# Performance work log

Measured on AMD Instinct MI355X. Metric: run time of the kernel, lower is better.

The kernel has to match this reference:

```python
import jax, jax.numpy as jnp
import numpy as np

N_SPK, N_UTT, D_EMB = 1024, 20, 512
COS_EPS = 1e-8   # torch F.cosine_similarity default eps
SIM_EPS = 1e-6   # added to cosine and inside the log, per original code


def setup_inputs() -> dict:
    key = jax.random.key(0)
    embeddings = jax.random.normal(key, (N_SPK, N_UTT, D_EMB), dtype=jnp.float32)
    w = jnp.asarray(10.0, dtype=jnp.float32)
    b = jnp.asarray(-5.0, dtype=jnp.float32)
    return {"embeddings": embeddings, "w": w, "b": b}


def reference(embeddings, w, b):
    N, M, D = embeddings.shape
    sums = embeddings.sum(axis=1)                       # [N, D]
    centroids = sums / M                                # [N, D] full centroids
    cent_excl = (sums[:, None, :] - embeddings) / (M - 1)  # [N, M, D] leave-one-out

    def _norm(x):
        return x / jnp.maximum(jnp.linalg.norm(x, axis=-1, keepdims=True), COS_EPS)

    e_n = _norm(embeddings)          # [N, M, D]
    c_n = _norm(centroids)           # [N, D]
    ce_n = _norm(cent_excl)          # [N, M, D]

    # cosine vs every speaker centroid
    cs = jnp.einsum('nmd,kd->nmk', e_n, c_n)            # [N, M, N]
    # replace same-speaker column with leave-one-out cosine
    diag = jnp.sum(e_n * ce_n, axis=-1)                 # [N, M]
    same = jnp.eye(N, dtype=bool)[:, None, :]           # [N, 1, N]
    cossim = jnp.where(same, diag[:, :, None], cs) + SIM_EPS

    sim = w * cossim + b                                # [N, M, N]
    pos = w * (diag + SIM_EPS) + b                      # sim[j, i, j]
    lse = jnp.log(jnp.sum(jnp.exp(sim), axis=-1) + SIM_EPS)  # [N, M]
    loss = jnp.sum(lse - pos)
    return loss
```

## Files before the change

### kernel.cpp

```cpp
#include <hip/hip_runtime.h>
#include <hip/hip_bf16.h>

typedef unsigned short u16;
typedef unsigned int u32;
typedef unsigned char u8;
typedef int i32x8 __attribute__((ext_vector_type(8)));
typedef float f32x4 __attribute__((ext_vector_type(4)));

#define NSPK 1024
#define NUTT 20
#define DEMB 512
#define NROW (NSPK * NUTT)

__device__ __forceinline__ uint2 pk_fp8x8(float a, float b, float c, float d,
                                          float e, float f, float g, float h) {
    int lo = __builtin_amdgcn_cvt_pk_fp8_f32(a, b, 0, 0);
    lo = __builtin_amdgcn_cvt_pk_fp8_f32(c, d, lo, 1);
    int hi = __builtin_amdgcn_cvt_pk_fp8_f32(e, f, 0, 0);
    hi = __builtin_amdgcn_cvt_pk_fp8_f32(g, h, hi, 1);
    return make_uint2((u32)lo, (u32)hi);
}

__global__ __launch_bounds__(256) void prep_f(const float* __restrict__ E,
                                              u8* __restrict__ A,
                                              u8* __restrict__ Bc,
                                              float* __restrict__ diag,
                                              float* __restrict__ csd,
                                              float* __restrict__ out) {
    __shared__ float sbuf[4][DEMB];
    const int t = threadIdx.x, lane = t & 63, wv = t >> 6;
    const int n = blockIdx.x;
    const float* Eb = E + (size_t)n * (NUTT * DEMB) + (size_t)(wv * 5) * DEMB + lane * 8;

    float4 e0[5], e1[5];
    float4 p0 = {0, 0, 0, 0}, p1 = {0, 0, 0, 0};
#pragma unroll
    for (int i = 0; i < 5; ++i) {
        e0[i] = *(const float4*)(Eb + (size_t)i * DEMB);
        e1[i] = *(const float4*)(Eb + (size_t)i * DEMB + 4);
        p0.x += e0[i].x; p0.y += e0[i].y; p0.z += e0[i].z; p0.w += e0[i].w;
        p1.x += e1[i].x; p1.y += e1[i].y; p1.z += e1[i].z; p1.w += e1[i].w;
    }
    *(float4*)(&sbuf[wv][lane * 8])     = p0;
    *(float4*)(&sbuf[wv][lane * 8 + 4]) = p1;
    __syncthreads();

    float4 s0 = {0, 0, 0, 0}, s1 = {0, 0, 0, 0};
#pragma unroll
    for (int k = 0; k < 4; ++k) {
        float4 a = *(const float4*)(&sbuf[k][lane * 8]);
        float4 b = *(const float4*)(&sbuf[k][lane * 8 + 4]);
        s0.x += a.x; s0.y += a.y; s0.z += a.z; s0.w += a.w;
        s1.x += b.x; s1.y += b.y; s1.z += b.z; s1.w += b.w;
    }

    float ls = s0.x*s0.x + s0.y*s0.y + s0.z*s0.z + s0.w*s0.w
             + s1.x*s1.x + s1.y*s1.y + s1.z*s1.z + s1.w*s1.w;
#pragma unroll
    for (int o = 32; o; o >>= 1) ls += __shfl_xor(ls, o);
    const float ss = ls;
    const float rc = 1.0f / fmaxf(sqrtf(ss) * 0.05f, 1e-8f);
    const float g  = rc * 0.05f;

    ((uint2*)(Bc + (size_t)n * DEMB))[lane] =
        pk_fp8x8(s0.x * g, s0.y * g, s0.z * g, s0.w * g,
                 s1.x * g, s1.y * g, s1.z * g, s1.w * g);

#pragma unroll
    for (int i = 0; i < 5; ++i) {
        float ee = e0[i].x*e0[i].x + e0[i].y*e0[i].y + e0[i].z*e0[i].z + e0[i].w*e0[i].w
                 + e1[i].x*e1[i].x + e1[i].y*e1[i].y + e1[i].z*e1[i].z + e1[i].w*e1[i].w;
        float es = e0[i].x*s0.x + e0[i].y*s0.y + e0[i].z*s0.z + e0[i].w*s0.w
                 + e1[i].x*s1.x + e1[i].y*s1.y + e1[i].z*s1.z + e1[i].w*s1.w;
#pragma unroll
        for (int o = 32; o; o >>= 1) { ee += __shfl_xor(ee, o); es += __shfl_xor(es, o); }

        const float rne = 1.0f / fmaxf(sqrtf(ee), 1e-8f);
        const float pxx = ss - 2.f * es + ee;
        const float dg  = (es - ee) * rne / fmaxf(sqrtf(pxx), 1.9e-7f);

        const int r = n * NUTT + wv * 5 + i;
        ((uint2*)(A + (size_t)r * DEMB))[lane] =
            pk_fp8x8(e0[i].x * rne, e0[i].y * rne, e0[i].z * rne, e0[i].w * rne,
                     e1[i].x * rne, e1[i].y * rne, e1[i].z * rne, e1[i].w * rne);
        if (lane == 0) {
            diag[r] = dg;
            csd[r]  = es * g * rne;
        }
    }

    if (n == 0 && t == 0) out[0] = 0.f;
}

__device__ __forceinline__ void async_copy16(const void* g, void* l) {
    __builtin_amdgcn_global_load_lds(
        (const __attribute__((address_space(1))) void*)g,
        (__attribute__((address_space(3))) void*)l, 16, 0, 0);
}

__global__ __launch_bounds__(256, 1) void gemm_fin(const u8* __restrict__ A,
                                                   const u8* __restrict__ Bc,
                                                   const float* __restrict__ wp,
                                                   const float* __restrict__ bp,
                                                   const float* __restrict__ diag,
                                                   const float* __restrict__ csd,
                                                   float* __restrict__ out) {
    __shared__ u8 As[80 * DEMB];
    __shared__ u8 Bls[4][2][4096];
    __shared__ float red[4][80];
    __shared__ float s_red[4];
    const int t = threadIdx.x, lane = t & 63, wv = t >> 6;
    const int ml = lane & 15, q = lane >> 4;
    const int blk = blockIdx.x;
    const u8* Ag = A + (size_t)blk * 80 * DEMB;

    const float w = *wp, bb = *bp;

#pragma unroll
    for (int jj = 0; jj < 10; ++jj) {
        const int c = t + 256 * jj;
        const int r = c >> 5, sl = c & 31;
        async_copy16(Ag + (size_t)r * DEMB + ((sl ^ (r & 31)) << 4),
                     As + t * 16 + jj * 4096);
    }

    const int C0 = wv * 256;
    int rj[4], kg16[4];
#pragma unroll
    for (int j = 0; j < 4; ++j) {
        const int c = lane + 64 * j;
        rj[j] = c >> 3;
        kg16[j] = ((c & 7) ^ (rj[j] & 7)) << 4;
    }

#define STAGEB(U, KT, PAR)                                                    \
    {                                                                         \
        _Pragma("unroll")                                                     \
        for (int j = 0; j < 4; ++j)                                           \
            async_copy16(Bc + (size_t)(C0 + (U) * 32 + rj[j]) * DEMB +        \
                             (KT) * 128 + kg16[j],                            \
                         &Bls[wv][PAR][j * 1024 + lane * 16]);                \
    }

    STAGEB(0, 0, 0);
    STAGEB(0, 1, 1);
    asm volatile("s_waitcnt vmcnt(8)" ::: "memory");
    __builtin_amdgcn_sched_barrier(0);
    __builtin_amdgcn_s_barrier();
    __builtin_amdgcn_sched_barrier(0);

    i32x8 a[5][4];
#pragma unroll
    for (int m = 0; m < 5; ++m) {
        const int r = m * 16 + ml;
#pragma unroll
        for (int kt = 0; kt < 4; ++kt) {
            const int sl0 = (kt * 8 + 2 * q)     ^ (r & 31);
            const int sl1 = (kt * 8 + 2 * q + 1) ^ (r & 31);
            uint4 x = *(const uint4*)(As + r * DEMB + (sl0 << 4));
            uint4 y = *(const uint4*)(As + r * DEMB + (sl1 << 4));
            a[m][kt] = (i32x8){(int)x.x, (int)x.y, (int)x.z, (int)x.w,
                               (int)y.x, (int)y.y, (int)y.z, (int)y.w};
        }
    }

    f32x4 acc[5][2], rowpart[5];
#pragma unroll
    for (int m = 0; m < 5; ++m) {
        acc[m][0] = (f32x4){0.f, 0.f, 0.f, 0.f};
        acc[m][1] = (f32x4){0.f, 0.f, 0.f, 0.f};
        rowpart[m] = (f32x4){0.f, 0.f, 0.f, 0.f};
    }

    int bo0[2], bo1[2];
#pragma unroll
    for (int nf = 0; nf < 2; ++nf) {
        const int cc = nf * 16 + ml;
        bo0[nf] = cc * 128 + (((2 * q)     ^ (cc & 7)) << 4);
        bo1[nf] = cc * 128 + (((2 * q + 1) ^ (cc & 7)) << 4);
    }

    i32x8 bf[2][2];
#define LOADBF(PAR)                                                           \
    {                                                                         \
        _Pragma("unroll")                                                     \
        for (int nf = 0; nf < 2; ++nf) {                                      \
            uint4 x = *(const uint4*)(&Bls[wv][PAR][bo0[nf]]);                \
            uint4 y = *(const uint4*)(&Bls[wv][PAR][bo1[nf]]);                \
            bf[PAR][nf] = (i32x8){(int)x.x, (int)x.y, (int)x.z, (int)x.w,     \
                                  (int)y.x, (int)y.y, (int)y.z, (int)y.w};    \
        }                                                                     \
    }

    asm volatile("s_waitcnt vmcnt(4)" ::: "memory");
    __builtin_amdgcn_sched_barrier(0);
    LOADBF(0);

#pragma unroll
    for (int u = 0; u < 8; ++u) {
#pragma unroll
        for (int kt = 0; kt < 4; ++kt) {
            const int s = u * 4 + kt, par = s & 1;
            asm volatile("s_waitcnt lgkmcnt(0)" ::: "memory");
            __builtin_amdgcn_sched_barrier(0);
            if (s + 2 < 32) {
                const int s2 = s + 2;
                STAGEB(s2 >> 2, s2 & 3, par);
            }
            __builtin_amdgcn_sched_barrier(0);
            if (s == 30)      { asm volatile("s_waitcnt vmcnt(0)" ::: "memory"); }
            else if (s < 30)  { asm volatile("s_waitcnt vmcnt(4)" ::: "memory"); }
            __builtin_amdgcn_sched_barrier(0);
            if (s < 31) LOADBF(par ^ 1);
#pragma unroll
            for (int m = 0; m < 5; ++m)
#pragma unroll
                for (int nf = 0; nf < 2; ++nf)
                    acc[m][nf] = __builtin_amdgcn_mfma_scale_f32_16x16x128_f8f6f4(
                        a[m][kt], bf[par][nf], acc[m][nf], 0, 0,
                        0, 0x7F7F7F7F, 0, 0x7F7F7F7F);
            if (kt == 3) {
#pragma unroll
                for (int m = 0; m < 5; ++m) {
#pragma unroll
                    for (int r = 0; r < 4; ++r)
                        rowpart[m][r] += __expf(fmaf(w, acc[m][0][r] + 1e-6f, bb))
                                       + __expf(fmaf(w, acc[m][1][r] + 1e-6f, bb));
                    acc[m][0] = (f32x4){0.f, 0.f, 0.f, 0.f};
                    acc[m][1] = (f32x4){0.f, 0.f, 0.f, 0.f};
                }
            }
        }
    }
#undef STAGEB
#undef LOADBF

#pragma unroll
    for (int m = 0; m < 5; ++m)
#pragma unroll
        for (int o = 1; o < 16; o <<= 1) {
            rowpart[m][0] += __shfl_xor(rowpart[m][0], o);
            rowpart[m][1] += __shfl_xor(rowpart[m][1], o);
            rowpart[m][2] += __shfl_xor(rowpart[m][2], o);
            rowpart[m][3] += __shfl_xor(rowpart[m][3], o);
        }
    if (ml == 0) {
#pragma unroll
        for (int m = 0; m < 5; ++m)
#pragma unroll
            for (int r = 0; r < 4; ++r)
                red[wv][m * 16 + q * 4 + r] = rowpart[m][r];
    }
    __syncthreads();

    float term = 0.f;
    if (t < 80) {
        const float rsum = red[0][t] + red[1][t] + red[2][t] + red[3][t];
        const int row = blk * 80 + t;
        const float pos = fmaf(w, diag[row] + 1e-6f, bb);
        const float S = rsum - __expf(fmaf(w, csd[row] + 1e-6f, bb)) + __expf(pos);
        term = __logf(S + 1e-6f) - pos;
    }
#pragma unroll
    for (int o = 32; o; o >>= 1) term += __shfl_xor(term, o);
    if (lane == 0) s_red[wv] = term;
    __syncthreads();
    if (t == 0) atomicAdd(out, s_red[0] + s_red[1] + s_red[2] + s_red[3]);
}

extern "C" void kernel_launch(void* const* d_in, const int* in_sizes, int n_in,
                              void* d_out, int out_size, void* d_ws, size_t ws_size,
                              hipStream_t stream) {
    const float* E = (const float*)d_in[0];
    const float* wp = (const float*)d_in[1];
    const float* bp = (const float*)d_in[2];
    float* out = (float*)d_out;

    char* ws = (char*)d_ws;
    u8* A      = (u8*)(ws);
    u8* Bc     = (u8*)(ws + 10485760);
    float* dg  = (float*)(ws + 11010048);
    float* cs  = (float*)(ws + 11091968);

    prep_f<<<NSPK, 256, 0, stream>>>(E, A, Bc, dg, cs, out);
    gemm_fin<<<256, 256, 0, stream>>>(A, Bc, wp, bp, dg, cs, out);
}
```

Baseline: 105.2 us.

## Triple-buffer B tiles and ping-pong accumulators to overlap exp epilogue with MFMA

Raises the per-wave B LDS staging from double to triple buffering, so loads run three k-steps ahead, and adjusts the vmcnt waits to match. The accumulators are split into two sets that alternate per column chunk. The exp/log-sum-exp fold of the previous chunk is spread across the four k-steps of the next chunk, so it can interleave with the MFMAs instead of stalling after each chunk. This costs more LDS and 40 more accumulator registers, which could hurt occupancy or cause spills.

```diff
diff --git a/kernel.cpp b/kernel.cpp
--- a/kernel.cpp
+++ b/kernel.cpp
@@ -106,7 +106,7 @@
                                                    const float* __restrict__ csd,
                                                    float* __restrict__ out) {
     __shared__ u8 As[80 * DEMB];
-    __shared__ u8 Bls[4][2][4096];
+    __shared__ u8 Bls[4][3][4096];
     __shared__ float red[4][80];
     __shared__ float s_red[4];
     const int t = threadIdx.x, lane = t & 63, wv = t >> 6;
@@ -133,18 +133,19 @@
         kg16[j] = ((c & 7) ^ (rj[j] & 7)) << 4;
     }
 
-#define STAGEB(U, KT, PAR)                                                    \
+#define STAGEB(U, KT, BI)                                                     \
     {                                                                         \
         _Pragma("unroll")                                                     \
         for (int j = 0; j < 4; ++j)                                           \
             async_copy16(Bc + (size_t)(C0 + (U) * 32 + rj[j]) * DEMB +        \
                              (KT) * 128 + kg16[j],                            \
-                         &Bls[wv][PAR][j * 1024 + lane * 16]);                \
+                         &Bls[wv][BI][j * 1024 + lane * 16]);                 \
     }
 
     STAGEB(0, 0, 0);
     STAGEB(0, 1, 1);
-    asm volatile("s_waitcnt vmcnt(8)" ::: "memory");
+    STAGEB(0, 2, 2);
+    asm volatile("s_waitcnt vmcnt(12)" ::: "memory");
     __builtin_amdgcn_sched_barrier(0);
     __builtin_amdgcn_s_barrier();
     __builtin_amdgcn_sched_barrier(0);
@@ -164,11 +165,13 @@
         }
     }
 
-    f32x4 acc[5][2], rowpart[5];
+    f32x4 accA[5][2], accB[5][2], rowpart[5];
 #pragma unroll
     for (int m = 0; m < 5; ++m) {
-        acc[m][0] = (f32x4){0.f, 0.f, 0.f, 0.f};
-        acc[m][1] = (f32x4){0.f, 0.f, 0.f, 0.f};
+        accA[m][0] = (f32x4){0.f, 0.f, 0.f, 0.f};
+        accA[m][1] = (f32x4){0.f, 0.f, 0.f, 0.f};
+        accB[m][0] = (f32x4){0.f, 0.f, 0.f, 0.f};
+        accB[m][1] = (f32x4){0.f, 0.f, 0.f, 0.f};
         rowpart[m] = (f32x4){0.f, 0.f, 0.f, 0.f};
     }
 
@@ -181,20 +184,32 @@
     }
 
     i32x8 bf[2][2];
-#define LOADBF(PAR)                                                           \
+#define LOADBF(BI, PAR)                                                       \
     {                                                                         \
         _Pragma("unroll")                                                     \
         for (int nf = 0; nf < 2; ++nf) {                                      \
-            uint4 x = *(const uint4*)(&Bls[wv][PAR][bo0[nf]]);                \
-            uint4 y = *(const uint4*)(&Bls[wv][PAR][bo1[nf]]);                \
+            uint4 x = *(const uint4*)(&Bls[wv][BI][bo0[nf]]);                 \
+            uint4 y = *(const uint4*)(&Bls[wv][BI][bo1[nf]]);                 \
             bf[PAR][nf] = (i32x8){(int)x.x, (int)x.y, (int)x.z, (int)x.w,     \
                                   (int)y.x, (int)y.y, (int)y.z, (int)y.w};    \
         }                                                                     \
     }
 
-    asm volatile("s_waitcnt vmcnt(4)" ::: "memory");
+#define FOLD(P, LO, HI)                                                       \
+    {                                                                         \
+        _Pragma("unroll")                                                     \
+        for (int e = (LO); e < (HI); ++e) {                                   \
+            const int fm = e >> 1, fn = e & 1;                                \
+            _Pragma("unroll")                                                 \
+            for (int r = 0; r < 4; ++r)                                       \
+                rowpart[fm][r] += __expf(fmaf(w, P[fm][fn][r] + 1e-6f, bb));  \
+            P[fm][fn] = (f32x4){0.f, 0.f, 0.f, 0.f};                          \
+        }                                                                     \
+    }
+
+    asm volatile("s_waitcnt vmcnt(8)" ::: "memory");
     __builtin_amdgcn_sched_barrier(0);
-    LOADBF(0);
+    LOADBF(0, 0);
 
 #pragma unroll
     for (int u = 0; u < 8; ++u) {
@@ -203,37 +218,35 @@
             const int s = u * 4 + kt, par = s & 1;
             asm volatile("s_waitcnt lgkmcnt(0)" ::: "memory");
             __builtin_amdgcn_sched_barrier(0);
-            if (s + 2 < 32) {
-                const int s2 = s + 2;
-                STAGEB(s2 >> 2, s2 & 3, par);
+            if (s + 3 < 32) {
+                STAGEB((s + 3) >> 2, (s + 3) & 3, s % 3);
             }
             __builtin_amdgcn_sched_barrier(0);
-            if (s == 30)      { asm volatile("s_waitcnt vmcnt(0)" ::: "memory"); }
-            else if (s < 30)  { asm volatile("s_waitcnt vmcnt(4)" ::: "memory"); }
+            if (s <= 28)      { asm volatile("s_waitcnt vmcnt(8)" ::: "memory"); }
+            else if (s == 29) { asm volatile("s_waitcnt vmcnt(4)" ::: "memory"); }
+            else if (s == 30) { asm volatile("s_waitcnt vmcnt(0)" ::: "memory"); }
             __builtin_amdgcn_sched_barrier(0);
-            if (s < 31) LOADBF(par ^ 1);
-#pragma unroll
-            for (int m = 0; m < 5; ++m)
-#pragma unroll
-                for (int nf = 0; nf < 2; ++nf)
-                    acc[m][nf] = __builtin_amdgcn_mfma_scale_f32_16x16x128_f8f6f4(
-                        a[m][kt], bf[par][nf], acc[m][nf], 0, 0,
-                        0, 0x7F7F7F7F, 0, 0x7F7F7F7F);
-            if (kt == 3) {
-#pragma unroll
-                for (int m = 0; m < 5; ++m) {
-#pragma unroll
-                    for (int r = 0; r < 4; ++r)
-                        rowpart[m][r] += __expf(fmaf(w, acc[m][0][r] + 1e-6f, bb))
-                                       + __expf(fmaf(w, acc[m][1][r] + 1e-6f, bb));
-                    acc[m][0] = (f32x4){0.f, 0.f, 0.f, 0.f};
-                    acc[m][1] = (f32x4){0.f, 0.f, 0.f, 0.f};
-                }
+            if (s < 31) LOADBF((s + 1) % 3, par ^ 1);
+            {
+                f32x4 (&C)[5][2] = (u & 1) ? accB : accA;
+#pragma unroll
+                for (int m = 0; m < 5; ++m)
+#pragma unroll
+                    for (int nf = 0; nf < 2; ++nf)
+                        C[m][nf] = __builtin_amdgcn_mfma_scale_f32_16x16x128_f8f6f4(
+                            a[m][kt], bf[par][nf], C[m][nf], 0, 0,
+                            0, 0x7F7F7F7F, 0, 0x7F7F7F7F);
+            }
+            if (u > 0) {
+                f32x4 (&P)[5][2] = (u & 1) ? accA : accB;
+                FOLD(P, kt * 3, (kt * 3 + 3 > 10) ? 10 : kt * 3 + 3);
             }
         }
     }
+    FOLD(accB, 0, 10);
 #undef STAGEB
 #undef LOADBF
+#undef FOLD
 
 #pragma unroll
     for (int m = 0; m < 5; ++m)
```

Measured after the change: 105.3 us. No clear change (+0.1%).
